# Kernel optimization log

Measured on AMD Instinct MI355X. Metric: run time of the kernel, lower is better.

## Reference

```python
import jax, jax.numpy as jnp
import numpy as np

OFFSET = 1e-6   # undefined global in source; small positive stabilizer
COS_EPS = 1e-8  # F.cosine_similarity default eps

B, N, M = 128, 2048, 128


def setup_inputs() -> dict:
    key = jax.random.key(0)
    ks = jax.random.split(key, 9)
    return {
        "memory": jax.random.normal(ks[0], (B, N, M), jnp.float32),
        "k_t": jax.random.normal(ks[1], (B, M), jnp.float32),
        "beta_t": jax.random.uniform(ks[2], (B,), jnp.float32),
        "g_t": jax.random.uniform(ks[3], (B,), jnp.float32),
        "w_t_minus_1": jax.random.uniform(ks[4], (B, N), jnp.float32),
        "s_t": jax.random.uniform(ks[5], (B, 3), jnp.float32),
        "gamma_t": jax.random.uniform(ks[6], (B,), jnp.float32),
        "e_t": jax.random.uniform(ks[7], (B, M), jnp.float32),
        "a_t": jax.random.normal(ks[8], (B, M), jnp.float32),
    }


def reference(memory, k_t, beta_t, g_t, w_t_minus_1, s_t, gamma_t, e_t, a_t):
    # ---- content_addressing (faithful to source, incl. w_tilde_t = w_{t-1} quirk) ----
    mk = memory + OFFSET                     # [B,N,M]
    kk = k_t[:, None, :] + OFFSET            # [B,1,M]
    dot = jnp.sum(mk * kk, axis=-1)          # [B,N]
    nm = jnp.maximum(jnp.sqrt(jnp.sum(mk * mk, -1)), COS_EPS)            # [B,N]
    nk = jnp.maximum(jnp.sqrt(jnp.sum(kk * kk, -1)), COS_EPS)            # [B,1]
    K = dot / (nm * nk)                      # cosine similarity, [B,N]
    w_c = jax.nn.softmax(beta_t[:, None] * K, axis=1)                    # [B,N]
    w_g = g_t[:, None] * w_c + (1.0 - g_t[:, None]) * w_t_minus_1        # [B,N]
    w_pow = w_t_minus_1 ** gamma_t[:, None]                              # sharpening on w_{t-1}
    w_t = jnp.sum(w_pow, axis=1, keepdims=True) + OFFSET                 # [B,1]
    w_t = jnp.broadcast_to(w_t, w_t_minus_1.shape)                       # [B,N] (source .repeat)

    # ---- writing: rank-1 erase/add memory update ----
    erase = w_t[:, :, None] * e_t[:, None, :]                            # [B,N,M]
    M_new = memory * (1.0 - erase) + w_t[:, :, None] * a_t[:, None, :]   # [B,N,M]

    # ---- reading ----
    r_t = jnp.einsum('bn,bnm->bm', w_t, M_new)                           # [B,M]

    # single concatenated output so every chain stays live: [B, M + 2N]
    return jnp.concatenate([r_t, w_t, w_g], axis=1)
```

## Files before the change

kernel.cpp:

```cpp
#include <hip/hip_runtime.h>
#include <hip/hip_bf16.h>
#include <math.h>

#define BB 128
#define NN 2048
#define MM 128
#define ROWS 128
#define CHUNKS (NN / ROWS)
#define STRIDE (MM + 4)
#define OFFSET_EPS 1e-6f
#define COS_EPS 1e-8f

__global__ __launch_bounds__(256) void pass_a(
    const float* __restrict__ memory, const float* __restrict__ k_t,
    const float* __restrict__ beta_t, float* __restrict__ colsum_part,
    float* __restrict__ score)
{
    __shared__ float tile[ROWS * STRIDE];
    __shared__ float ks[MM];
    __shared__ float s_col[8][MM];
    __shared__ float s_bon;
    __shared__ float s_epsK1;

    const int b     = blockIdx.x / CHUNKS;
    const int chunk = blockIdx.x % CHUNKS;
    const int r0    = chunk * ROWS;
    const int t     = threadIdx.x;

    if (t < 32) {
        float4 kv = *(const float4*)(k_t + b * MM + 4 * t);
        const float e0 = kv.x + OFFSET_EPS, e1 = kv.y + OFFSET_EPS,
                    e2 = kv.z + OFFSET_EPS, e3 = kv.w + OFFSET_EPS;
        *(float4*)&ks[4 * t] = make_float4(e0, e1, e2, e3);
        float s2 = e0 * e0 + e1 * e1 + e2 * e2 + e3 * e3;
        float s1 = e0 + e1 + e2 + e3;
        #pragma unroll
        for (int s = 16; s; s >>= 1) {
            s2 += __shfl_xor(s2, s);
            s1 += __shfl_xor(s1, s);
        }
        if (t == 0) {
            s_bon   = beta_t[b] / fmaxf(sqrtf(s2), COS_EPS);
            s_epsK1 = OFFSET_EPS * s1;
        }
    }

    const float* src = memory + (size_t)(b * NN + r0) * MM;
    float cs0 = 0.f, cs1 = 0.f, cs2 = 0.f, cs3 = 0.f;
    #pragma unroll
    for (int i = 0; i < 16; ++i) {
        float4 v = *(const float4*)(src + i * 1024 + 4 * t);
        cs0 += v.x; cs1 += v.y; cs2 += v.z; cs3 += v.w;
        const int row = i * 8 + (t >> 5);
        const int col = (4 * t) & 127;
        *(float4*)&tile[row * STRIDE + col] = v;
    }
    *(float4*)&s_col[t >> 5][(4 * t) & 127] = make_float4(cs0, cs1, cs2, cs3);
    __syncthreads();

    const int r = t >> 1;
    const int h = t & 1;
    const float* vrow = &tile[r * STRIDE + h * 64];
    const float* krow = &ks[h * 64];
    float dot = 0.f, sq = 0.f, rs = 0.f;
    #pragma unroll
    for (int j = 0; j < 16; ++j) {
        float4 v = *(const float4*)(vrow + 4 * j);
        float4 k = *(const float4*)(krow + 4 * j);
        dot += v.x * k.x + v.y * k.y + v.z * k.z + v.w * k.w;
        sq  += v.x * v.x + v.y * v.y + v.z * v.z + v.w * v.w;
        rs  += v.x + v.y + v.z + v.w;
    }
    dot += __shfl_xor(dot, 1);
    sq  += __shfl_xor(sq, 1);
    rs  += __shfl_xor(rs, 1);
    if (h == 0) {
        const float d   = dot + s_epsK1;
        const float nm2 = sq + 2.0f * OFFSET_EPS * rs
                          + (float)MM * OFFSET_EPS * OFFSET_EPS;
        const float nm  = fmaxf(sqrtf(nm2), COS_EPS);
        score[b * NN + r0 + r] = d * s_bon / nm;
    }

    if (t < MM) {
        float v = 0.f;
        #pragma unroll
        for (int g = 0; g < 8; ++g) v += s_col[g][t];
        colsum_part[(size_t)chunk * (BB * MM) + b * MM + t] = v;
    }
}

__global__ __launch_bounds__(256) void pass_b(
    const float* __restrict__ score,  const float* __restrict__ g_t,
    const float* __restrict__ w_prev, const float* __restrict__ gamma_t,
    const float* __restrict__ e_t,    const float* __restrict__ a_t,
    const float* __restrict__ colsum_part, float* __restrict__ out)
{
    const int b   = blockIdx.x;
    const int tid = threadIdx.x;
    __shared__ float red[256];

    float sc[8];
    float mx = -INFINITY;
    #pragma unroll
    for (int i = 0; i < 8; ++i) {
        sc[i] = score[b * NN + tid + 256 * i];
        mx = fmaxf(mx, sc[i]);
    }
    red[tid] = mx; __syncthreads();
    for (int s = 128; s; s >>= 1) {
        if (tid < s) red[tid] = fmaxf(red[tid], red[tid + s]);
        __syncthreads();
    }
    mx = red[0]; __syncthreads();

    float sum = 0.f;
    #pragma unroll
    for (int i = 0; i < 8; ++i) {
        sc[i] = __expf(sc[i] - mx);
        sum += sc[i];
    }
    red[tid] = sum; __syncthreads();
    for (int s = 128; s; s >>= 1) {
        if (tid < s) red[tid] += red[tid + s];
        __syncthreads();
    }
    const float inv_sum = 1.f / red[0];
    __syncthreads();

    const float g     = g_t[b];
    const float gamma = gamma_t[b];
    float wg[8];
    float psum = 0.f;
    #pragma unroll
    for (int i = 0; i < 8; ++i) {
        const float w = w_prev[b * NN + tid + 256 * i];
        wg[i] = g * (sc[i] * inv_sum) + (1.f - g) * w;
        psum += __powf(w, gamma);
    }
    red[tid] = psum; __syncthreads();
    for (int s = 128; s; s >>= 1) {
        if (tid < s) red[tid] += red[tid + s];
        __syncthreads();
    }
    const float S = red[0] + OFFSET_EPS;

    float* orow = out + (size_t)b * (MM + 2 * NN);
    #pragma unroll
    for (int i = 0; i < 8; ++i) {
        const int n = tid + 256 * i;
        orow[MM + n]      = S;
        orow[MM + NN + n] = wg[i];
    }
    if (tid < MM) {
        float cs = 0.f;
        #pragma unroll
        for (int c = 0; c < CHUNKS; ++c)
            cs += colsum_part[(size_t)c * (BB * MM) + b * MM + tid];
        const float r = S * ((1.f - S * e_t[b * MM + tid]) * cs +
                             (float)NN * S * a_t[b * MM + tid]);
        orow[tid] = r;
    }
}

extern "C" void kernel_launch(void* const* d_in, const int* in_sizes, int n_in,
                              void* d_out, int out_size, void* d_ws, size_t ws_size,
                              hipStream_t stream) {
    const float* memory  = (const float*)d_in[0];
    const float* k_t     = (const float*)d_in[1];
    const float* beta_t  = (const float*)d_in[2];
    const float* g_t     = (const float*)d_in[3];
    const float* w_prev  = (const float*)d_in[4];
    const float* gamma_t = (const float*)d_in[6];
    const float* e_t     = (const float*)d_in[7];
    const float* a_t     = (const float*)d_in[8];
    float* out = (float*)d_out;

    float* colsum_part = (float*)d_ws;
    float* score       = colsum_part + CHUNKS * BB * MM;

    const int grid_a = BB * CHUNKS;
    pass_a<<<grid_a, 256, 0, stream>>>(memory, k_t, beta_t, colsum_part, score);
    pass_b<<<BB, 256, 0, stream>>>(score, g_t, w_prev, gamma_t, e_t, a_t,
                                   colsum_part, out);
}
```

Measured before the change: 213.2 us.

## Fuse softmax/write pass into scoring kernel via last-block atomic counter

Merges the two kernels into one: each chunk block increments a per-batch counter after writing its scores and column sums, and the last block for a batch does the softmax, gating, sharpening sum and read output. The separate max reduction is dropped because scores are bounded cosine values times beta, and the block reductions now use wave shuffles. This removes one kernel launch and the serialized second grid, but adds a memset launch, thread fences and an atomic per block. Skipping the max subtraction could overflow if beta is large.

```diff
diff --git a/kernel.cpp b/kernel.cpp
--- a/kernel.cpp
+++ b/kernel.cpp
@@ -11,16 +11,21 @@
 #define OFFSET_EPS 1e-6f
 #define COS_EPS 1e-8f
 
-__global__ __launch_bounds__(256) void pass_a(
+__global__ __launch_bounds__(256) void fused(
     const float* __restrict__ memory, const float* __restrict__ k_t,
-    const float* __restrict__ beta_t, float* __restrict__ colsum_part,
-    float* __restrict__ score)
+    const float* __restrict__ beta_t, const float* __restrict__ g_t,
+    const float* __restrict__ w_prev, const float* __restrict__ gamma_t,
+    const float* __restrict__ e_t,    const float* __restrict__ a_t,
+    float* __restrict__ colsum_part,  float* __restrict__ score,
+    unsigned int* __restrict__ done,  float* __restrict__ out)
 {
     __shared__ float tile[ROWS * STRIDE];
     __shared__ float ks[MM];
     __shared__ float s_col[8][MM];
     __shared__ float s_bon;
     __shared__ float s_epsK1;
+    __shared__ unsigned int s_flag;
+    __shared__ float s_red[8];
 
     const int b     = blockIdx.x / CHUNKS;
     const int chunk = blockIdx.x % CHUNKS;
@@ -88,78 +93,53 @@
         for (int g = 0; g < 8; ++g) v += s_col[g][t];
         colsum_part[(size_t)chunk * (BB * MM) + b * MM + t] = v;
     }
-}
 
-__global__ __launch_bounds__(256) void pass_b(
-    const float* __restrict__ score,  const float* __restrict__ g_t,
-    const float* __restrict__ w_prev, const float* __restrict__ gamma_t,
-    const float* __restrict__ e_t,    const float* __restrict__ a_t,
-    const float* __restrict__ colsum_part, float* __restrict__ out)
-{
-    const int b   = blockIdx.x;
-    const int tid = threadIdx.x;
-    __shared__ float red[256];
-
-    float sc[8];
-    float mx = -INFINITY;
-    #pragma unroll
-    for (int i = 0; i < 8; ++i) {
-        sc[i] = score[b * NN + tid + 256 * i];
-        mx = fmaxf(mx, sc[i]);
-    }
-    red[tid] = mx; __syncthreads();
-    for (int s = 128; s; s >>= 1) {
-        if (tid < s) red[tid] = fmaxf(red[tid], red[tid + s]);
-        __syncthreads();
-    }
-    mx = red[0]; __syncthreads();
-
-    float sum = 0.f;
-    #pragma unroll
-    for (int i = 0; i < 8; ++i) {
-        sc[i] = __expf(sc[i] - mx);
-        sum += sc[i];
-    }
-    red[tid] = sum; __syncthreads();
-    for (int s = 128; s; s >>= 1) {
-        if (tid < s) red[tid] += red[tid + s];
-        __syncthreads();
-    }
-    const float inv_sum = 1.f / red[0];
+    __threadfence();
     __syncthreads();
+    if (t == 0) s_flag = atomicAdd(&done[b], 1u);
+    __syncthreads();
+    if (s_flag != CHUNKS - 1) return;
+    __threadfence();
 
     const float g     = g_t[b];
     const float gamma = gamma_t[b];
-    float wg[8];
-    float psum = 0.f;
+    float ex[8], wv[8];
+    float esum = 0.f, psum = 0.f;
     #pragma unroll
     for (int i = 0; i < 8; ++i) {
-        const float w = w_prev[b * NN + tid + 256 * i];
-        wg[i] = g * (sc[i] * inv_sum) + (1.f - g) * w;
-        psum += __powf(w, gamma);
+        const int n = t + 256 * i;
+        ex[i] = __expf(score[b * NN + n]);
+        esum += ex[i];
+        wv[i] = w_prev[b * NN + n];
+        psum += __powf(wv[i], gamma);
     }
-    red[tid] = psum; __syncthreads();
-    for (int s = 128; s; s >>= 1) {
-        if (tid < s) red[tid] += red[tid + s];
-        __syncthreads();
+    #pragma unroll
+    for (int s = 32; s; s >>= 1) {
+        esum += __shfl_xor(esum, s);
+        psum += __shfl_xor(psum, s);
     }
-    const float S = red[0] + OFFSET_EPS;
+    const int wave = t >> 6;
+    const int lane = t & 63;
+    if (lane == 0) { s_red[wave] = esum; s_red[4 + wave] = psum; }
+    __syncthreads();
+    const float inv_sum = 1.f / (s_red[0] + s_red[1] + s_red[2] + s_red[3]);
+    const float S = (s_red[4] + s_red[5] + s_red[6] + s_red[7]) + OFFSET_EPS;
 
     float* orow = out + (size_t)b * (MM + 2 * NN);
     #pragma unroll
     for (int i = 0; i < 8; ++i) {
-        const int n = tid + 256 * i;
+        const int n = t + 256 * i;
         orow[MM + n]      = S;
-        orow[MM + NN + n] = wg[i];
+        orow[MM + NN + n] = g * ex[i] * inv_sum + (1.f - g) * wv[i];
     }
-    if (tid < MM) {
+    if (t < MM) {
         float cs = 0.f;
         #pragma unroll
         for (int c = 0; c < CHUNKS; ++c)
-            cs += colsum_part[(size_t)c * (BB * MM) + b * MM + tid];
-        const float r = S * ((1.f - S * e_t[b * MM + tid]) * cs +
-                             (float)NN * S * a_t[b * MM + tid]);
-        orow[tid] = r;
+            cs += colsum_part[(size_t)c * (BB * MM) + b * MM + t];
+        const float rr = S * ((1.f - S * e_t[b * MM + t]) * cs +
+                              (float)NN * S * a_t[b * MM + t]);
+        orow[t] = rr;
     }
 }
 
@@ -178,9 +158,11 @@
 
     float* colsum_part = (float*)d_ws;
     float* score       = colsum_part + CHUNKS * BB * MM;
+    unsigned int* done = (unsigned int*)(score + BB * NN);
 
-    const int grid_a = BB * CHUNKS;
-    pass_a<<<grid_a, 256, 0, stream>>>(memory, k_t, beta_t, colsum_part, score);
-    pass_b<<<BB, 256, 0, stream>>>(score, g_t, w_prev, gamma_t, e_t, a_t,
-                                   colsum_part, out);
+    hipMemsetAsync(done, 0, BB * sizeof(unsigned int), stream);
+
+    fused<<<BB * CHUNKS, 256, 0, stream>>>(memory, k_t, beta_t, g_t, w_prev,
+                                           gamma_t, e_t, a_t,
+                                           colsum_part, score, done, out);
 }
```

Measured after the change: 588.4 us. +176.0%, slower.
